# Kernel optimization log

Hardware: AMD Instinct MI355X
Metric: run time of the kernel (lower is better)

## Reference

```python
import jax, jax.numpy as jnp
import numpy as np

NUM_HEADS = 16


def setup_inputs() -> dict:
    key = jax.random.key(0)
    ks = jax.random.split(key, 6)
    B, N, M, C = 2, 2048, 2048, 1024
    return {
        "reference_data": jax.random.normal(ks[0], (B, N, C), dtype=jnp.float32),
        "target_data": jax.random.normal(ks[1], (B, M, C), dtype=jnp.float32),
        "Wq": jax.random.normal(ks[2], (C, C), dtype=jnp.float32) * (C ** -0.5),
        "Wkv": jax.random.normal(ks[3], (C, 2 * C), dtype=jnp.float32) * (C ** -0.5),
        "Wproj": jax.random.normal(ks[4], (C, C), dtype=jnp.float32) * (C ** -0.5),
        "bproj": jnp.zeros((C,), dtype=jnp.float32),
    }


def reference(reference_data, target_data, Wq, Wkv, Wproj, bproj):
    B, N, C = reference_data.shape
    M = target_data.shape[1]
    H = NUM_HEADS
    hd = C // H
    scale = hd ** -0.5
    # k, v from reference: [B, N, 2, H, hd] -> two [B, H, N, hd]
    kv = (reference_data @ Wkv).reshape(B, N, 2, H, hd)
    k = jnp.transpose(kv[:, :, 0], (0, 2, 1, 3))  # [B,H,N,hd]
    v = jnp.transpose(kv[:, :, 1], (0, 2, 1, 3))  # [B,H,N,hd]
    # q from target: [B, H, M, hd]
    q = jnp.transpose((target_data @ Wq).reshape(B, M, H, hd), (0, 2, 1, 3))
    attn = jnp.einsum("bhid,bhjd->bhij", q, k) * scale  # [B,H,M,N]
    attn = jax.nn.softmax(attn, axis=-1)
    x = jnp.einsum("bhij,bhjd->bhid", attn, v)  # [B,H,M,hd]
    x = jnp.transpose(x, (0, 2, 1, 3)).reshape(B, M, C)
    return x @ Wproj + bproj
```

## Files before the change

kernel.cpp:

```cpp
#include <hip/hip_runtime.h>
#include <hip/hip_bf16.h>
#include <stdint.h>

#define SEQ   2048
#define CH    1024
#define NH    16
#define HD    64

typedef short bf8 __attribute__((ext_vector_type(8)));
typedef short bf4 __attribute__((ext_vector_type(4)));
typedef float f4  __attribute__((ext_vector_type(4)));
typedef unsigned short u16;

#define GAS(p) ((const __attribute__((address_space(1))) void*)(p))
#define LAS(p) ((__attribute__((address_space(3))) void*)(p))

__device__ __forceinline__ u16 f2bf(float f) {
  uint32_t u = __float_as_uint(f);
  u += 0x7fffu + ((u >> 16) & 1u);
  return (u16)(u >> 16);
}

__device__ __forceinline__ float bf2f(u16 v) {
  return __uint_as_float(((uint32_t)v) << 16);
}

__device__ __forceinline__ uint32_t pk2bf(float a, float b) {
  float2 f; f.x = a; f.y = b;
  __hip_bfloat162 h = __float22bfloat162_rn(f);
  union { __hip_bfloat162 h; uint32_t u; } cv; cv.h = h;
  return cv.u;
}

__device__ __forceinline__ float fexp2(float x) {
#if __has_builtin(__builtin_amdgcn_exp2f)
  return __builtin_amdgcn_exp2f(x);
#else
  return exp2f(x);
#endif
}

__device__ __forceinline__ f4 MFMA32(bf8 a, bf8 b, f4 c) {
  return __builtin_amdgcn_mfma_f32_16x16x32_bf16(a, b, c, 0, 0, 0);
}

__device__ __forceinline__ f4 MFMA16(bf4 a, bf4 b, f4 c) {
#if __has_builtin(__builtin_amdgcn_mfma_f32_16x16x16_bf16)
  return __builtin_amdgcn_mfma_f32_16x16x16_bf16(a, b, c, 0, 0, 0);
#elif __has_builtin(__builtin_amdgcn_mfma_f32_16x16x16bf16_1k)
  return __builtin_amdgcn_mfma_f32_16x16x16bf16_1k(a, b, c, 0, 0, 0);
#else
  f4 d = c;
  asm volatile("v_mfma_f32_16x16x16_bf16 %0, %1, %2, %0"
               : "+v"(d) : "v"(a), "v"(b));
  return d;
#endif
}

__global__ void prep(const float* __restrict__ ref, u16* __restrict__ refb,
                     const float* __restrict__ tgt, u16* __restrict__ tgtb,
                     const float* __restrict__ Wq, u16* __restrict__ Wqt,
                     const float* __restrict__ Wkv, u16* __restrict__ Wkvt,
                     const float* __restrict__ Wp, u16* __restrict__ Wpt) {
  __shared__ float tile[32][33];
  int blk = blockIdx.x;
  int t = threadIdx.x;
  if (blk < 8192) {
    const float* in; u16* out;
    if (blk < 4096) { in = ref; out = refb; } else { in = tgt; out = tgtb; blk -= 4096; }
    int i = (blk * 256 + t) * 4;
    float4 f = *reinterpret_cast<const float4*>(in + i);
    ushort4 o;
    o.x = f2bf(f.x); o.y = f2bf(f.y); o.z = f2bf(f.z); o.w = f2bf(f.w);
    *reinterpret_cast<ushort4*>(out + i) = o;
    return;
  }
  blk -= 8192;
  int x = blk & 127, by = blk >> 7;
  const float* in; u16* out; int N;
  if (x < 32)       { in = Wq;  out = Wqt;  N = CH;     }
  else if (x < 96)  { in = Wkv; out = Wkvt; N = 2 * CH; x -= 32; }
  else              { in = Wp;  out = Wpt;  N = CH;     x -= 96; }
  const int K = CH;
  int bn = x * 32, bk = by * 32;
  int tx = t & 31, ty = t >> 5;
  #pragma unroll
  for (int i = ty; i < 32; i += 8)
    tile[i][tx] = in[(size_t)(bk + i) * N + bn + tx];
  __syncthreads();
  #pragma unroll
  for (int i = ty; i < 32; i += 8)
    out[(size_t)(bn + i) * K + bk + tx] = f2bf(tile[tx][i]);
}

__global__ __launch_bounds__(256, 3)
void gemm_qkv(const u16* __restrict__ tgtb, const u16* __restrict__ refb,
              const u16* __restrict__ Wqt, const u16* __restrict__ Wkvt,
              u16* __restrict__ qb, u16* __restrict__ karr, u16* __restrict__ varr)
{
  __shared__ __align__(16) u16 As[2][4096];
  __shared__ __align__(16) u16 Bs[2][4096];
  const int tid = threadIdx.x;
  const int lane = tid & 63, wave = tid >> 6;
  const int l16 = lane & 15, q = lane >> 4;
  const bool isQ = blockIdx.x >= 16;
  const u16* A  = isQ ? tgtb : refb;
  const u16* Bt = isQ ? Wqt : Wkvt;
  const int n0 = (isQ ? (blockIdx.x - 16) : blockIdx.x) * 128;
  const int m0 = blockIdx.y * 128;
  const int wm = (wave >> 1) * 64, wn = (wave & 1) * 64;
  const int Kdim = CH;
  const int c = tid, c2 = tid + 256;
  const int ar = c >> 2, ac = (c & 3) << 3, ar2 = c2 >> 2, ac2 = (c2 & 3) << 3;

  f4 acc[4][4] = {};

  #define STAGE_G(buf, k0)                                                      \
    { __builtin_amdgcn_global_load_lds(                                         \
          GAS(&A[(size_t)(m0 + ar) * Kdim + (k0) + ac]),                        \
          LAS(&As[buf][c << 3]), 16, 0, 0);                                     \
      __builtin_amdgcn_global_load_lds(                                         \
          GAS(&A[(size_t)(m0 + ar2) * Kdim + (k0) + ac2]),                      \
          LAS(&As[buf][c2 << 3]), 16, 0, 0);                                    \
      __builtin_amdgcn_global_load_lds(                                         \
          GAS(&Bt[(size_t)(n0 + ar) * Kdim + (k0) + ac]),                       \
          LAS(&Bs[buf][c << 3]), 16, 0, 0);                                     \
      __builtin_amdgcn_global_load_lds(                                         \
          GAS(&Bt[(size_t)(n0 + ar2) * Kdim + (k0) + ac2]),                     \
          LAS(&Bs[buf][c2 << 3]), 16, 0, 0); }

  STAGE_G(0, 0);
  for (int kk = 0; kk < 32; ++kk) {
    __syncthreads();
    if (kk < 31) STAGE_G((kk + 1) & 1, (kk + 1) * 32);
    const u16* as = As[kk & 1];
    const u16* bs = Bs[kk & 1];
    bf8 a[4], b[4];
    #pragma unroll
    for (int i = 0; i < 4; ++i)
      a[i] = *reinterpret_cast<const bf8*>(&as[(wm + i * 16 + l16) * 32 + q * 8]);
    #pragma unroll
    for (int j = 0; j < 4; ++j)
      b[j] = *reinterpret_cast<const bf8*>(&bs[(wn + j * 16 + l16) * 32 + q * 8]);
    #pragma unroll
    for (int i = 0; i < 4; ++i)
      #pragma unroll
      for (int j = 0; j < 4; ++j)
        acc[i][j] = MFMA32(a[i], b[j], acc[i][j]);
  }
  #undef STAGE_G

  #pragma unroll
  for (int i = 0; i < 4; ++i) {
    const int mbase = m0 + wm + i * 16 + q * 4;
    const int b = mbase >> 11, ns0 = mbase & (SEQ - 1);
    #pragma unroll
    for (int j = 0; j < 4; ++j) {
      const int n = n0 + wn + j * 16 + l16;
      if (isQ) {
        int h = n >> 6, d = n & 63;
        #pragma unroll
        for (int r = 0; r < 4; ++r)
          qb[(size_t)((b * NH + h) * SEQ + ns0 + r) * HD + d] =
              f2bf(acc[i][j][r] * 0.1803368801f);
      } else if (n < CH) {
        int h = n >> 6, d = n & 63;
        size_t base = (size_t)(b * NH + h) * SEQ * HD;
        int off = (((ns0 >> 4) * 2 + (d >> 5)) * 4 + ((d >> 3) & 3)) * 128
                  + (d & 7);
        #pragma unroll
        for (int r = 0; r < 4; ++r)
          karr[base + off + ((ns0 + r) & 15) * 8] = f2bf(acc[i][j][r]);
      } else {
        int c2v = n - CH, h = c2v >> 6, d = c2v & 63;
        size_t base = (size_t)(b * NH + h) * SEQ * HD;
        int off = (((ns0 >> 4) * 2 + (d >> 5)) * 4 + ((ns0 >> 2) & 3)) * 128
                  + (d & 15) * 8 + ((d >> 4) & 1) * 4;
        ushort4 st;
        st.x = f2bf(acc[i][j][0]); st.y = f2bf(acc[i][j][1]);
        st.z = f2bf(acc[i][j][2]); st.w = f2bf(acc[i][j][3]);
        *reinterpret_cast<ushort4*>(&varr[base + off]) = st;
      }
    }
  }
}

__global__ __launch_bounds__(256, 2)
void gemm_proj(const u16* __restrict__ A, const u16* __restrict__ Bt,
               float* __restrict__ fo, const float* __restrict__ bias)
{
  __shared__ __align__(16) u16 As[2][2048];
  __shared__ __align__(16) u16 Bs[2][4096];
  const int tid = threadIdx.x;
  const int lane = tid & 63, wave = tid >> 6;
  const int l16 = lane & 15, q = lane >> 4;
  const int m0 = blockIdx.y * 64, n0 = blockIdx.x * 128;
  const int wm = (wave >> 1) * 32, wn = (wave & 1) * 64;
  const int Kdim = CH;
  const int c = tid, c2 = tid + 256;
  const int ar = c >> 2, ac = (c & 3) << 3, ar2 = c2 >> 2, ac2 = (c2 & 3) << 3;

  f4 acc[2][4] = {};

  const int aar = c >> 2;
  const int aac = (c & 3) << 3;
  #define STAGE_P(buf, k0)                                                      \
    { __builtin_amdgcn_global_load_lds(                                         \
          GAS(&A[(size_t)(m0 + aar) * Kdim + (k0) + aac]),                      \
          LAS(&As[buf][c << 3]), 16, 0, 0);                                     \
      __builtin_amdgcn_global_load_lds(                                         \
          GAS(&Bt[(size_t)(n0 + ar) * Kdim + (k0) + ac]),                       \
          LAS(&Bs[buf][c << 3]), 16, 0, 0);                                     \
      __builtin_amdgcn_global_load_lds(                                         \
          GAS(&Bt[(size_t)(n0 + ar2) * Kdim + (k0) + ac2]),                     \
          LAS(&Bs[buf][c2 << 3]), 16, 0, 0); }

  STAGE_P(0, 0);
  for (int kk = 0; kk < 32; ++kk) {
    __syncthreads();
    if (kk < 31) STAGE_P((kk + 1) & 1, (kk + 1) * 32);
    const u16* as = As[kk & 1];
    const u16* bs = Bs[kk & 1];
    bf8 a[2], b[4];
    #pragma unroll
    for (int i = 0; i < 2; ++i)
      a[i] = *reinterpret_cast<const bf8*>(&as[(wm + i * 16 + l16) * 32 + q * 8]);
    #pragma unroll
    for (int j = 0; j < 4; ++j)
      b[j] = *reinterpret_cast<const bf8*>(&bs[(wn + j * 16 + l16) * 32 + q * 8]);
    #pragma unroll
    for (int i = 0; i < 2; ++i)
      #pragma unroll
      for (int j = 0; j < 4; ++j)
        acc[i][j] = MFMA32(a[i], b[j], acc[i][j]);
  }
  #undef STAGE_P

  #pragma unroll
  for (int i = 0; i < 2; ++i) {
    const int mbase = m0 + wm + i * 16 + q * 4;
    #pragma unroll
    for (int j = 0; j < 4; ++j) {
      const int n = n0 + wn + j * 16 + l16;
      #pragma unroll
      for (int r = 0; r < 4; ++r)
        fo[(size_t)(mbase + r) * CH + n] = acc[i][j][r] + bias[n];
    }
  }
}

__global__ __launch_bounds__(256, 4)
void attn(const u16* __restrict__ Q, const u16* __restrict__ Karr,
          const u16* __restrict__ Varr, u16* __restrict__ XP,
          float* __restrict__ DS)
{
  __shared__ __align__(16) u16 Ks[2][4096];
  __shared__ __align__(16) u16 Vs[2][4096];
  const int tid = threadIdx.x;
  const int lane = tid & 63;
  const int l16 = lane & 15, q = lane >> 4;
  const int bh = blockIdx.y;
  const int z = blockIdx.z;
  const int m0 = blockIdx.x * 128;
  const int wm = (tid >> 6) * 32;

  const u16* Qb = Q    + (size_t)bh * SEQ * HD;
  const u16* Kb = Karr + (size_t)bh * SEQ * HD + (size_t)z * 1024 * HD;
  const u16* Vb = Varr + (size_t)bh * SEQ * HD + (size_t)z * 1024 * HD;

  bf8 qf[2][2];
  #pragma unroll
  for (int g = 0; g < 2; ++g)
    #pragma unroll
    for (int s = 0; s < 2; ++s)
      qf[g][s] = *reinterpret_cast<const bf8*>(
          &Qb[(size_t)(m0 + wm + g * 16 + l16) * HD + s * 32 + q * 8]);

  const short one_bf = 0x3F80;
  const bf4 ones = {one_bf, one_bf, one_bf, one_bf};

  f4 o[2][4] = {};
  f4 ds[2] = {};

  #define STAGE_A(buf, t)                                                      \
    { __builtin_amdgcn_global_load_lds(GAS(Kb + (size_t)(t) * 4096 + tid * 8), \
                                       LAS(&Ks[buf][tid * 8]), 16, 0, 0);      \
      __builtin_amdgcn_global_load_lds(GAS(Kb + (size_t)(t) * 4096 + 2048 + tid * 8), \
                                       LAS(&Ks[buf][2048 + tid * 8]), 16, 0, 0); \
      __builtin_amdgcn_global_load_lds(GAS(Vb + (size_t)(t) * 4096 + tid * 8), \
                                       LAS(&Vs[buf][tid * 8]), 16, 0, 0);      \
      __builtin_amdgcn_global_load_lds(GAS(Vb + (size_t)(t) * 4096 + 2048 + tid * 8), \
                                       LAS(&Vs[buf][2048 + tid * 8]), 16, 0, 0); }

  STAGE_A(0, 0);
  for (int t = 0; t < 16; ++t) {
    __syncthreads();
    if (t < 15) STAGE_A((t + 1) & 1, t + 1);
    const u16* ks = Ks[t & 1];
    const u16* vs = Vs[t & 1];

    bf4 pa[2][4];
    #pragma unroll
    for (int j = 0; j < 4; ++j) {
      bf8 kf0 = *reinterpret_cast<const bf8*>(&ks[((j * 2 + 0) * 4 + q) * 128 + l16 * 8]);
      bf8 kf1 = *reinterpret_cast<const bf8*>(&ks[((j * 2 + 1) * 4 + q) * 128 + l16 * 8]);
      #pragma unroll
      for (int g = 0; g < 2; ++g) {
        f4 zf = {};
        zf = MFMA32(kf0, qf[g][0], zf);
        zf = MFMA32(kf1, qf[g][1], zf);
        union { bf4 v; uint32_t u[2]; } w;
        w.u[0] = pk2bf(fexp2(zf[0]), fexp2(zf[1]));
        w.u[1] = pk2bf(fexp2(zf[2]), fexp2(zf[3]));
        pa[g][j] = w.v;
      }
    }

    #pragma unroll
    for (int j = 0; j < 4; ++j) {
      ds[0] = MFMA16(pa[0][j], ones, ds[0]);
      ds[1] = MFMA16(pa[1][j], ones, ds[1]);
      #pragma unroll
      for (int dh = 0; dh < 2; ++dh) {
        bf8 vv = *reinterpret_cast<const bf8*>(&vs[((j * 2 + dh) * 4 + q) * 128 + l16 * 8]);
        bf4 v0 = __builtin_shufflevector(vv, vv, 0, 1, 2, 3);
        bf4 v1 = __builtin_shufflevector(vv, vv, 4, 5, 6, 7);
        #pragma unroll
        for (int g = 0; g < 2; ++g) {
          o[g][dh * 2 + 0] = MFMA16(pa[g][j], v0, o[g][dh * 2 + 0]);
          o[g][dh * 2 + 1] = MFMA16(pa[g][j], v1, o[g][dh * 2 + 1]);
        }
      }
    }
  }
  #undef STAGE_A

  #pragma unroll
  for (int g = 0; g < 2; ++g) {
    #pragma unroll
    for (int r = 0; r < 4; ++r) {
      float ir = 1.0f / ds[g][r];
      int m = m0 + wm + g * 16 + q * 4 + r;
      size_t row = (size_t)(z * NH * 2 + bh) * SEQ + m;
      if (l16 == 0) DS[row] = ds[g][r];
      #pragma unroll
      for (int dt = 0; dt < 4; ++dt) {
        int d = dt * 16 + l16;
        XP[row * HD + d] = f2bf(o[g][dt][r] * ir);
      }
    }
  }
}

__global__ __launch_bounds__(256)
void combine(const u16* __restrict__ XP, const float* __restrict__ DS,
             u16* __restrict__ xb)
{
  const int t = threadIdx.x;
  const int row = blockIdx.x * 16 + (t >> 4);
  const int d0 = (t & 15) * 4;
  const float s0 = DS[row], s1 = DS[65536 + row];
  const float inv = 1.0f / (s0 + s1);
  const float w0 = s0 * inv, w1 = s1 * inv;
  ushort4 a = *reinterpret_cast<const ushort4*>(&XP[(size_t)row * HD + d0]);
  ushort4 b4 = *reinterpret_cast<const ushort4*>(
      &XP[(size_t)(65536 + row) * HD + d0]);
  ushort4 o;
  o.x = f2bf(w0 * bf2f(a.x) + w1 * bf2f(b4.x));
  o.y = f2bf(w0 * bf2f(a.y) + w1 * bf2f(b4.y));
  o.z = f2bf(w0 * bf2f(a.z) + w1 * bf2f(b4.z));
  o.w = f2bf(w0 * bf2f(a.w) + w1 * bf2f(b4.w));
  const int bh = row >> 11, m = row & (SEQ - 1);
  const int b = bh >> 4, h = bh & (NH - 1);
  *reinterpret_cast<ushort4*>(
      &xb[(size_t)(b * SEQ + m) * CH + h * HD + d0]) = o;
}

extern "C" void kernel_launch(void* const* d_in, const int* in_sizes, int n_in,
                              void* d_out, int out_size, void* d_ws, size_t ws_size,
                              hipStream_t stream) {
  const float* ref   = (const float*)d_in[0];
  const float* tgt   = (const float*)d_in[1];
  const float* Wq    = (const float*)d_in[2];
  const float* Wkv   = (const float*)d_in[3];
  const float* Wproj = (const float*)d_in[4];
  const float* bproj = (const float*)d_in[5];
  float* out = (float*)d_out;

  char* ws = (char*)d_ws;
  u16* refb = (u16*)(ws);
  u16* tgtb = (u16*)(ws + (8  << 20));
  u16* Wqt  = (u16*)(ws + (16 << 20));
  u16* Wkvt = (u16*)(ws + (18 << 20));
  u16* Wpt  = (u16*)(ws + (22 << 20));
  u16* qb   = (u16*)(ws + (24 << 20));
  u16* karr = (u16*)(ws + (32 << 20));
  u16* varr = (u16*)(ws + (40 << 20));
  u16* xb   = (u16*)(ws + (48 << 20));
  u16*   XP = (u16*)(ws);
  float* DS = (float*)(ws + (16 << 20));

  prep<<<12288, 256, 0, stream>>>(ref, refb, tgt, tgtb, Wq, Wqt, Wkv, Wkvt, Wproj, Wpt);

  gemm_qkv<<<dim3(24, 32), 256, 0, stream>>>(tgtb, refb, Wqt, Wkvt, qb, karr, varr);

  attn<<<dim3(16, 32, 2), 256, 0, stream>>>(qb, karr, varr, XP, DS);

  combine<<<4096, 256, 0, stream>>>(XP, DS, xb);

  gemm_proj<<<dim3(8, 64), 256, 0, stream>>>(xb, Wpt, out, bproj);
}
```

Baseline: 208.2 us.

## Drop split-KV attention and combine kernel, write attention output directly

Removes the two-way split of the key/value sequence across blockIdx.z. Each attention block now loops over all 32 KV tiles and writes normalized bf16 output straight into the [B,M,C] layout, so the separate combine kernel and its partial-result and denominator buffers go away. This saves one launch and the global round trip of the partials. In exchange the grid halves to 512 blocks, which reduces parallelism and latency hiding on a many-CU GPU, and each block's serial loop doubles.

```diff
diff --git a/kernel.cpp b/kernel.cpp
--- a/kernel.cpp
+++ b/kernel.cpp
@@ -19,10 +19,6 @@
   uint32_t u = __float_as_uint(f);
   u += 0x7fffu + ((u >> 16) & 1u);
   return (u16)(u >> 16);
-}
-
-__device__ __forceinline__ float bf2f(u16 v) {
-  return __uint_as_float(((uint32_t)v) << 16);
 }
 
 __device__ __forceinline__ uint32_t pk2bf(float a, float b) {
@@ -251,8 +247,7 @@
 
 __global__ __launch_bounds__(256, 4)
 void attn(const u16* __restrict__ Q, const u16* __restrict__ Karr,
-          const u16* __restrict__ Varr, u16* __restrict__ XP,
-          float* __restrict__ DS)
+          const u16* __restrict__ Varr, u16* __restrict__ X)
 {
   __shared__ __align__(16) u16 Ks[2][4096];
   __shared__ __align__(16) u16 Vs[2][4096];
@@ -260,13 +255,12 @@
   const int lane = tid & 63;
   const int l16 = lane & 15, q = lane >> 4;
   const int bh = blockIdx.y;
-  const int z = blockIdx.z;
   const int m0 = blockIdx.x * 128;
   const int wm = (tid >> 6) * 32;
 
   const u16* Qb = Q    + (size_t)bh * SEQ * HD;
-  const u16* Kb = Karr + (size_t)bh * SEQ * HD + (size_t)z * 1024 * HD;
-  const u16* Vb = Varr + (size_t)bh * SEQ * HD + (size_t)z * 1024 * HD;
+  const u16* Kb = Karr + (size_t)bh * SEQ * HD;
+  const u16* Vb = Varr + (size_t)bh * SEQ * HD;
 
   bf8 qf[2][2];
   #pragma unroll
@@ -293,9 +287,9 @@
                                        LAS(&Vs[buf][2048 + tid * 8]), 16, 0, 0); }
 
   STAGE_A(0, 0);
-  for (int t = 0; t < 16; ++t) {
+  for (int t = 0; t < 32; ++t) {
     __syncthreads();
-    if (t < 15) STAGE_A((t + 1) & 1, t + 1);
+    if (t < 31) STAGE_A((t + 1) & 1, t + 1);
     const u16* ks = Ks[t & 1];
     const u16* vs = Vs[t & 1];
 
@@ -335,45 +329,20 @@
   }
   #undef STAGE_A
 
+  const int b = bh >> 4, h = bh & (NH - 1);
   #pragma unroll
   for (int g = 0; g < 2; ++g) {
     #pragma unroll
     for (int r = 0; r < 4; ++r) {
       float ir = 1.0f / ds[g][r];
       int m = m0 + wm + g * 16 + q * 4 + r;
-      size_t row = (size_t)(z * NH * 2 + bh) * SEQ + m;
-      if (l16 == 0) DS[row] = ds[g][r];
       #pragma unroll
       for (int dt = 0; dt < 4; ++dt) {
         int d = dt * 16 + l16;
-        XP[row * HD + d] = f2bf(o[g][dt][r] * ir);
+        X[(size_t)(b * SEQ + m) * CH + h * HD + d] = f2bf(o[g][dt][r] * ir);
       }
     }
   }
-}
-
-__global__ __launch_bounds__(256)
-void combine(const u16* __restrict__ XP, const float* __restrict__ DS,
-             u16* __restrict__ xb)
-{
-  const int t = threadIdx.x;
-  const int row = blockIdx.x * 16 + (t >> 4);
-  const int d0 = (t & 15) * 4;
-  const float s0 = DS[row], s1 = DS[65536 + row];
-  const float inv = 1.0f / (s0 + s1);
-  const float w0 = s0 * inv, w1 = s1 * inv;
-  ushort4 a = *reinterpret_cast<const ushort4*>(&XP[(size_t)row * HD + d0]);
-  ushort4 b4 = *reinterpret_cast<const ushort4*>(
-      &XP[(size_t)(65536 + row) * HD + d0]);
-  ushort4 o;
-  o.x = f2bf(w0 * bf2f(a.x) + w1 * bf2f(b4.x));
-  o.y = f2bf(w0 * bf2f(a.y) + w1 * bf2f(b4.y));
-  o.z = f2bf(w0 * bf2f(a.z) + w1 * bf2f(b4.z));
-  o.w = f2bf(w0 * bf2f(a.w) + w1 * bf2f(b4.w));
-  const int bh = row >> 11, m = row & (SEQ - 1);
-  const int b = bh >> 4, h = bh & (NH - 1);
-  *reinterpret_cast<ushort4*>(
-      &xb[(size_t)(b * SEQ + m) * CH + h * HD + d0]) = o;
 }
 
 extern "C" void kernel_launch(void* const* d_in, const int* in_sizes, int n_in,
@@ -397,16 +366,12 @@
   u16* karr = (u16*)(ws + (32 << 20));
   u16* varr = (u16*)(ws + (40 << 20));
   u16* xb   = (u16*)(ws + (48 << 20));
-  u16*   XP = (u16*)(ws);
-  float* DS = (float*)(ws + (16 << 20));
 
   prep<<<12288, 256, 0, stream>>>(ref, refb, tgt, tgtb, Wq, Wqt, Wkv, Wkvt, Wproj, Wpt);
 
   gemm_qkv<<<dim3(24, 32), 256, 0, stream>>>(tgtb, refb, Wqt, Wkvt, qb, karr, varr);
 
-  attn<<<dim3(16, 32, 2), 256, 0, stream>>>(qb, karr, varr, XP, DS);
-
-  combine<<<4096, 256, 0, stream>>>(XP, DS, xb);
+  attn<<<dim3(16, 32), 256, 0, stream>>>(qb, karr, varr, xb);
 
   gemm_proj<<<dim3(8, 64), 256, 0, stream>>>(xb, Wpt, out, bproj);
 }
```

After: 209.6 us. About the same (+0.7%).
